# Kernel optimization log

Measured on AMD Instinct MI355X. Metric: run time of the kernel, lower is better.

The kernel has to match this reference:

```python
import jax, jax.numpy as jnp
import numpy as np

N = 50000      # nodes
E = 800000     # edges
F_IN = 128     # n_features
H = 4          # n_heads
C1 = 64        # n_hidden (per-head out of layer 1)
C2 = 32        # n_classes (per-head out of layer 2)
NEG_SLOPE = 0.2
EPS = 1e-16


def setup_inputs() -> dict:
    key = jax.random.key(0)
    ks = jax.random.split(key, 12)
    x = jax.random.normal(ks[0], (N, F_IN), dtype=jnp.float32)
    edge_index = jax.random.randint(ks[1], (2, E), 0, N, dtype=jnp.int64)
    # layer 1 params (GATConv: shared lin for src/dst, att_src/att_dst vectors, bias)
    W1 = jax.random.normal(ks[2], (F_IN, H * C1), dtype=jnp.float32) * (1.0 / np.sqrt(F_IN))
    att_src1 = jax.random.normal(ks[3], (H, C1), dtype=jnp.float32) * 0.1
    att_dst1 = jax.random.normal(ks[4], (H, C1), dtype=jnp.float32) * 0.1
    b1 = jnp.zeros((C1,), dtype=jnp.float32)
    # layer 2 params
    W2 = jax.random.normal(ks[5], (C1, H * C2), dtype=jnp.float32) * (1.0 / np.sqrt(C1))
    att_src2 = jax.random.normal(ks[6], (H, C2), dtype=jnp.float32) * 0.1
    att_dst2 = jax.random.normal(ks[7], (H, C2), dtype=jnp.float32) * 0.1
    b2 = jnp.zeros((C2,), dtype=jnp.float32)
    return {"x": x, "edge_index": edge_index,
            "W1": W1, "att_src1": att_src1, "att_dst1": att_dst1, "b1": b1,
            "W2": W2, "att_src2": att_src2, "att_dst2": att_dst2, "b2": b2}


def gat_conv(x, src, dst, W, att_src, att_dst, b, heads, out_ch):
    """PyG GATConv with concat=False (head-averaged output)."""
    n = x.shape[0]
    h = (x @ W).reshape(n, heads, out_ch)                 # [N, H, C]
    a_s = jnp.einsum('nhc,hc->nh', h, att_src)            # [N, H]
    a_d = jnp.einsum('nhc,hc->nh', h, att_dst)            # [N, H]
    e = jax.nn.leaky_relu(a_s[src] + a_d[dst], NEG_SLOPE)  # [E, H]
    # segment softmax over edges grouped by destination node
    m = jax.ops.segment_max(e, dst, num_segments=n)        # [N, H]
    m = jnp.where(jnp.isfinite(m), m, 0.0)
    ex = jnp.exp(e - m[dst])                               # [E, H]
    denom = jax.ops.segment_sum(ex, dst, num_segments=n)   # [N, H]
    alpha = ex / (denom[dst] + EPS)                        # [E, H]
    # scatter-add aggregation of attended source features
    msg = alpha[:, :, None] * h[src]                       # [E, H, C]
    out = jax.ops.segment_sum(msg, dst, num_segments=n)    # [N, H, C]
    return out.mean(axis=1) + b                            # [N, C]


def reference(x, edge_index, W1, att_src1, att_dst1, b1, W2, att_src2, att_dst2, b2):
    src, dst = edge_index[0], edge_index[1]
    h = jax.nn.relu(gat_conv(x, src, dst, W1, att_src1, att_dst1, b1, H, C1))
    # dropout is identity in eval mode
    out = gat_conv(h, src, dst, W2, att_src2, att_dst2, b2, H, C2)
    return out
```

## Files before the change

kernel.cpp:

```cpp
#include <hip/hip_runtime.h>
#include <hip/hip_fp16.h>
#include <cstdint>
#include <cstddef>

#define N_NODES 50000
#define N_EDGES 800000
#define F_IN 128
#define H_HEADS 4
#define C1 64
#define C2 32
#define NEG_SLOPE 0.2f
#define EPS_GAT 1e-16f
#define SLOT_CAP 96
#define FILL_BPG 256
#define NODES_PER_GROUP 6250
#define GEMM1_BLOCKS 782
#define CBASE ((int)0xAAAAAAAAu)

typedef _Float16 half8 __attribute__((ext_vector_type(8)));
typedef float f32x4 __attribute__((ext_vector_type(4)));

template<int K, int M>
__device__ __forceinline__ void wtrans_dev(const float* __restrict__ W,
                                           _Float16* __restrict__ Wt,
                                           _Float16* tile, int bm, int bk) {
    const int m0 = bm * 64, k0 = bk * 64;
    const int t = threadIdx.x;
    const int c = t & 63;
#pragma unroll
    for (int j = 0; j < 16; ++j) {
        int r = (t >> 6) + 4 * j;
        tile[c * 66 + r] = (_Float16)W[(size_t)(k0 + r) * M + m0 + c];
    }
    __syncthreads();
#pragma unroll
    for (int j = 0; j < 16; ++j) {
        int m_l = (t >> 6) + 4 * j;
        Wt[(size_t)(m0 + m_l) * K + k0 + c] = tile[m_l * 66 + c];
    }
}

__global__ __launch_bounds__(256) void wtrans_kernel(
        const float* __restrict__ W1, _Float16* __restrict__ wt1,
        const float* __restrict__ W2, _Float16* __restrict__ wt2) {
    __shared__ _Float16 tile[64 * 66];
    const int b = blockIdx.x;
    if (b < 8) {
        wtrans_dev<F_IN, H_HEADS * C1>(W1, wt1, tile, b & 3, b >> 2);
    } else {
        wtrans_dev<C1, H_HEADS * C2>(W2, wt2, tile, b - 8, 0);
    }
}

__device__ __forceinline__ void fill_dev(
        const int* __restrict__ src, const int* __restrict__ dst,
        int* __restrict__ cursor, unsigned short* __restrict__ slots,
        int fb) {
    const int g = (fb + (GEMM1_BLOCKS & 7)) & 7;
    const int bg = fb >> 3;
    const int dlo = g * NODES_PER_GROUP;
    const int dhi = dlo + NODES_PER_GROUP;
    const int4* dst4 = (const int4*)dst;
    const int4* src4 = (const int4*)src;
    constexpr int NV4 = N_EDGES / 4;
    for (int v = bg * 256 + (int)threadIdx.x; v < NV4; v += FILL_BPG * 256) {
        int4 d4 = dst4[v];
        int4 s4 = src4[v];
        if (d4.x >= dlo && d4.x < dhi) {
            unsigned int p = (unsigned int)(atomicAdd(&cursor[d4.x], 1) - CBASE);
            if (p < SLOT_CAP) slots[(size_t)d4.x * SLOT_CAP + p] = (unsigned short)s4.x;
        }
        if (d4.y >= dlo && d4.y < dhi) {
            unsigned int p = (unsigned int)(atomicAdd(&cursor[d4.y], 1) - CBASE);
            if (p < SLOT_CAP) slots[(size_t)d4.y * SLOT_CAP + p] = (unsigned short)s4.y;
        }
        if (d4.z >= dlo && d4.z < dhi) {
            unsigned int p = (unsigned int)(atomicAdd(&cursor[d4.z], 1) - CBASE);
            if (p < SLOT_CAP) slots[(size_t)d4.z * SLOT_CAP + p] = (unsigned short)s4.z;
        }
        if (d4.w >= dlo && d4.w < dhi) {
            unsigned int p = (unsigned int)(atomicAdd(&cursor[d4.w], 1) - CBASE);
            if (p < SLOT_CAP) slots[(size_t)d4.w * SLOT_CAP + p] = (unsigned short)s4.w;
        }
    }
}

template<int K, int M, int Hn, int C, typename InT>
__device__ __forceinline__ void gemm_att_dev(
        const InT* __restrict__ X, const _Float16* __restrict__ Wt,
        _Float16* __restrict__ Hout,
        const float* __restrict__ atts, const float* __restrict__ attd,
        float* __restrict__ as_, float* __restrict__ ad_, int Nr,
        _Float16* Ah, _Float16* Bt, _Float16* Ht, int row0) {
    constexpr int LDK = K + 8;
    constexpr int NCT = M / 64;
    constexpr int HPB = 64 / C;
    const int t = threadIdx.x;
    const int wv = t >> 6;
    const int lane = t & 63;
    const int quad = lane >> 4;
    const int n16 = lane & 15;

    if constexpr (sizeof(InT) == 4) {
        constexpr int KQ = K / 4;
#pragma unroll
        for (int j = 0; j < (64 * KQ) / 256; ++j) {
            int flat = t + 256 * j;
            int r = flat / KQ, kq = flat % KQ;
            int rg = row0 + r;
            float4 v = make_float4(0.f, 0.f, 0.f, 0.f);
            if (rg < Nr) v = *(const float4*)&X[(size_t)rg * K + 4 * kq];
            _Float16 tmp[4] = {(_Float16)v.x, (_Float16)v.y, (_Float16)v.z, (_Float16)v.w};
            *(uint2*)&Ah[r * LDK + 4 * kq] = *(const uint2*)tmp;
        }
    } else {
        constexpr int KQ = K / 8;
#pragma unroll
        for (int j = 0; j < (64 * KQ) / 256; ++j) {
            int flat = t + 256 * j;
            int r = flat / KQ, kq = flat % KQ;
            int rg = row0 + r;
            uint4 v = make_uint4(0u, 0u, 0u, 0u);
            if (rg < Nr) v = *(const uint4*)&X[(size_t)rg * K + 8 * kq];
            *(uint4*)&Ah[r * LDK + 8 * kq] = v;
        }
    }
    __syncthreads();

    half8 af[K / 32];
    const _Float16* Ap = &Ah[(16 * wv + n16) * LDK + 8 * quad];
#pragma unroll
    for (int ki = 0; ki < K / 32; ++ki) af[ki] = *(const half8*)(Ap + 32 * ki);

    for (int ct = 0; ct < NCT; ++ct) {
        const int col0 = 64 * ct;
        __syncthreads();
        {
            constexpr int KQ8 = K / 8;
#pragma unroll
            for (int j = 0; j < (64 * KQ8) / 256; ++j) {
                int flat = t + 256 * j;
                int c = flat / KQ8, kq = flat % KQ8;
                uint4 v = *(const uint4*)&Wt[(size_t)(col0 + c) * K + 8 * kq];
                *(uint4*)&Bt[c * LDK + 8 * kq] = v;
            }
        }
        __syncthreads();

        f32x4 acc[4];
#pragma unroll
        for (int nf = 0; nf < 4; ++nf) acc[nf] = (f32x4){0.f, 0.f, 0.f, 0.f};
#pragma unroll
        for (int ki = 0; ki < K / 32; ++ki) {
#pragma unroll
            for (int nf = 0; nf < 4; ++nf) {
                half8 bf = *(const half8*)&Bt[(16 * nf + n16) * LDK + 32 * ki + 8 * quad];
                acc[nf] = __builtin_amdgcn_mfma_f32_16x16x32_f16(af[ki], bf, acc[nf], 0, 0, 0);
            }
        }

        float dps[HPB][4], dpd[HPB][4];
#pragma unroll
        for (int u = 0; u < HPB; ++u)
#pragma unroll
            for (int r = 0; r < 4; ++r) { dps[u][r] = 0.f; dpd[u][r] = 0.f; }
#pragma unroll
        for (int nf = 0; nf < 4; ++nf) {
            int gc = col0 + 16 * nf + n16;
            float cs = atts[gc], cd = attd[gc];
#pragma unroll
            for (int r = 0; r < 4; ++r) {
                float av = acc[nf][r];
                dps[(16 * nf) / C][r] += av * cs;
                dpd[(16 * nf) / C][r] += av * cd;
            }
        }
#pragma unroll
        for (int u = 0; u < HPB; ++u)
#pragma unroll
            for (int r = 0; r < 4; ++r) {
                float s = dps[u][r], d = dpd[u][r];
#pragma unroll
                for (int off = 1; off < 16; off <<= 1) {
                    s += __shfl_xor(s, off, 64);
                    d += __shfl_xor(d, off, 64);
                }
                dps[u][r] = s; dpd[u][r] = d;
            }
        if (n16 == 0) {
            const int h0 = col0 / C;
#pragma unroll
            for (int r = 0; r < 4; ++r) {
                int row = row0 + 16 * wv + 4 * quad + r;
                if (row < Nr) {
#pragma unroll
                    for (int u = 0; u < HPB; ++u) {
                        as_[row * Hn + h0 + u] = dps[u][r];
                        ad_[row * Hn + h0 + u] = dpd[u][r];
                    }
                }
            }
        }

#pragma unroll
        for (int nf = 0; nf < 4; ++nf)
#pragma unroll
            for (int r = 0; r < 4; ++r)
                Ht[(16 * wv + 4 * quad + r) * 72 + 16 * nf + n16] = (_Float16)acc[nf][r];
        __syncthreads();
#pragma unroll
        for (int j = 0; j < 2; ++j) {
            int chunk = t + 256 * j;
            int r = chunk >> 3, cc = chunk & 7;
            int row = row0 + r;
            if (row < Nr) {
                uint4 v = *(const uint4*)&Ht[r * 72 + 8 * cc];
                *(uint4*)&Hout[(size_t)row * M + col0 + 8 * cc] = v;
            }
        }
    }
}

__global__ __launch_bounds__(256) void gemm1_fill_kernel(
        const float* __restrict__ x, const _Float16* __restrict__ wt1,
        _Float16* __restrict__ h1,
        const float* __restrict__ atts, const float* __restrict__ attd,
        float* __restrict__ as_, float* __restrict__ ad_,
        const int* __restrict__ src, const int* __restrict__ dst,
        int* __restrict__ cursor, unsigned short* __restrict__ slots) {
    constexpr int LDK = F_IN + 8;
    __shared__ _Float16 Ah[64 * LDK];
    __shared__ _Float16 Bt[64 * LDK];
    __shared__ _Float16 Ht[64 * 72];
    if (blockIdx.x < GEMM1_BLOCKS) {
        gemm_att_dev<F_IN, H_HEADS * C1, H_HEADS, C1, float>(
            x, wt1, h1, atts, attd, as_, ad_, N_NODES,
            Ah, Bt, Ht, blockIdx.x * 64);
    } else {
        fill_dev(src, dst, cursor, slots, blockIdx.x - GEMM1_BLOCKS);
    }
}

template<int K, int M, int Hn, int C, typename InT>
__global__ __launch_bounds__(256) void gemm_att_kernel(
        const InT* __restrict__ X, const _Float16* __restrict__ Wt,
        _Float16* __restrict__ Hout,
        const float* __restrict__ atts, const float* __restrict__ attd,
        float* __restrict__ as_, float* __restrict__ ad_, int Nr) {
    constexpr int LDK = K + 8;
    __shared__ _Float16 Ah[64 * LDK];
    __shared__ _Float16 Bt[64 * LDK];
    __shared__ _Float16 Ht[64 * 72];
    gemm_att_dev<K, M, Hn, C, InT>(X, Wt, Hout, atts, attd, as_, ad_, Nr,
                                   Ah, Bt, Ht, blockIdx.x * 64);
}

template<int Hn, int C, bool RELU, bool OUT_F16>
__global__ __launch_bounds__(256) void gat_agg_kernel(
        const int* __restrict__ degp, const unsigned short* __restrict__ slots,
        const float* __restrict__ as_, const float* __restrict__ ad_,
        const _Float16* __restrict__ Hm, const float* __restrict__ bias,
        void* __restrict__ outv, int Nr) {
    constexpr int HC = Hn * C;
    constexpr int PER = HC / 16;
    constexpr int NV = PER / 8;
    int node = blockIdx.x * 4 + (threadIdx.x >> 6);
    int lane = threadIdx.x & 63;
    if (node >= Nr) return;
    const int g = lane >> 4;
    const int l = lane & 15;
    const int h = l >> 2;
    const float ad_h = ad_[node * Hn + h];

    const int dn = min(degp[node] - CBASE, SLOT_CAP);
    const int begin = node * SLOT_CAP;
    const int end = begin + dn;
    const int iters = (dn + 3) >> 2;

    float acc[PER];
#pragma unroll
    for (int t = 0; t < PER; ++t) acc[t] = 0.f;
    float wsum = 0.f;

    int idx = begin + g;
    bool okA = idx < end;
    int sA = (int)slots[okA ? idx : begin];
    float aA = as_[sA * Hn + h];
    uint4 uA[NV];
    {
        const uint4* hp = (const uint4*)(Hm + (size_t)sA * HC + l * PER);
        uA[0] = hp[0];
        if constexpr (NV == 2) uA[1] = hp[1];
    }

#pragma unroll 2
    for (int it = 0; it < iters; ++it) {
        const int j = idx + 4;
        const bool okB = j < end;
        int sB = (int)slots[okB ? j : begin];
        float aB = as_[sB * Hn + h];
        uint4 uB[NV];
        {
            const uint4* hp = (const uint4*)(Hm + (size_t)sB * HC + l * PER);
            uB[0] = hp[0];
            if constexpr (NV == 2) uB[1] = hp[1];
        }

        float logit = aA + ad_h;
        float lr = fmaxf(logit, NEG_SLOPE * logit);
        float w = okA ? __expf(lr) : 0.f;
        wsum += w;
#pragma unroll
        for (int v = 0; v < NV; ++v) {
            half8 hv = __builtin_bit_cast(half8, uA[v]);
#pragma unroll
            for (int e = 0; e < 8; ++e)
                acc[8 * v + e] = fmaf((float)hv[e], w, acc[8 * v + e]);
        }

        okA = okB; aA = aB;
        uA[0] = uB[0];
        if constexpr (NV == 2) uA[1] = uB[1];
        idx = j;
    }

#pragma unroll
    for (int t = 0; t < PER; ++t) {
        acc[t] += __shfl_xor(acc[t], 16, 64);
        acc[t] += __shfl_xor(acc[t], 32, 64);
    }
    wsum += __shfl_xor(wsum, 16, 64);
    wsum += __shfl_xor(wsum, 32, 64);
    const float inv = 1.f / (wsum + EPS_GAT);
    float val[PER];
#pragma unroll
    for (int t = 0; t < PER; ++t) {
        float v = acc[t] * inv;
        v += __shfl_xor(v, 4, 64);
        v += __shfl_xor(v, 8, 64);
        val[t] = v * (1.0f / Hn);
    }
    if (lane < 4) {
        const int c0 = lane * PER;
#pragma unroll
        for (int t = 0; t < PER; ++t) {
            float v = val[t] + bias[c0 + t];
            if (RELU) v = fmaxf(v, 0.f);
            val[t] = v;
        }
        if constexpr (OUT_F16) {
            _Float16* o = (_Float16*)outv;
            _Float16 tmp[PER];
#pragma unroll
            for (int t = 0; t < PER; ++t) tmp[t] = (_Float16)val[t];
            uint4* d4 = (uint4*)&o[(size_t)node * C + c0];
            d4[0] = *(const uint4*)&tmp[0];
            if constexpr (NV == 2) d4[1] = *(const uint4*)&tmp[8];
        } else {
            float* o = (float*)outv;
#pragma unroll
            for (int t4 = 0; t4 < PER / 4; ++t4)
                *(float4*)&o[(size_t)node * C + c0 + 4 * t4] =
                    make_float4(val[4 * t4 + 0], val[4 * t4 + 1],
                                val[4 * t4 + 2], val[4 * t4 + 3]);
        }
    }
}

extern "C" void kernel_launch(void* const* d_in, const int* in_sizes, int n_in,
                              void* d_out, int out_size, void* d_ws, size_t ws_size,
                              hipStream_t stream) {
    const float* x    = (const float*)d_in[0];
    const int*   ei   = (const int*)d_in[1];
    const float* W1   = (const float*)d_in[2];
    const float* as1w = (const float*)d_in[3];
    const float* ad1w = (const float*)d_in[4];
    const float* b1   = (const float*)d_in[5];
    const float* W2   = (const float*)d_in[6];
    const float* as2w = (const float*)d_in[7];
    const float* ad2w = (const float*)d_in[8];
    const float* b2   = (const float*)d_in[9];
    float* out = (float*)d_out;

    const int* src = ei;
    const int* dst = ei + N_EDGES;

    char* ws = (char*)d_ws;
    size_t off = 0;
    auto alloc = [&](size_t bytes) -> void* {
        void* p = ws + off;
        off = (off + bytes + 255) & ~(size_t)255;
        return p;
    };
    int*   cursor = (int*)alloc((size_t)N_NODES * 4);
    float* as1_ = (float*)alloc((size_t)N_NODES * H_HEADS * 4);
    float* ad1_ = (float*)alloc((size_t)N_NODES * H_HEADS * 4);
    float* as2_ = (float*)alloc((size_t)N_NODES * H_HEADS * 4);
    float* ad2_ = (float*)alloc((size_t)N_NODES * H_HEADS * 4);
    _Float16* h1   = (_Float16*)alloc((size_t)N_NODES * H_HEADS * C1 * 2);
    _Float16* out1 = (_Float16*)alloc((size_t)N_NODES * C1 * 2);
    _Float16* h2   = (_Float16*)alloc((size_t)N_NODES * H_HEADS * C2 * 2);
    _Float16* wt1  = (_Float16*)alloc((size_t)(H_HEADS * C1) * F_IN * 2);
    _Float16* wt2  = (_Float16*)alloc((size_t)(H_HEADS * C2) * C1 * 2);
    unsigned short* slots = (unsigned short*)alloc((size_t)N_NODES * SLOT_CAP * 2);

    wtrans_kernel<<<10, 256, 0, stream>>>(W1, wt1, W2, wt2);

    gemm1_fill_kernel<<<GEMM1_BLOCKS + 8 * FILL_BPG, 256, 0, stream>>>(
        x, wt1, h1, as1w, ad1w, as1_, ad1_, src, dst, cursor, slots);

    gat_agg_kernel<H_HEADS, C1, true, true><<<(N_NODES + 3) / 4, 256, 0, stream>>>(
        cursor, slots, as1_, ad1_, h1, b1, (void*)out1, N_NODES);

    gemm_att_kernel<C1, H_HEADS * C2, H_HEADS, C2, _Float16>
        <<<GEMM1_BLOCKS, 256, 0, stream>>>(
            out1, wt2, h2, as2w, ad2w, as2_, ad2_, N_NODES);

    gat_agg_kernel<H_HEADS, C2, false, false><<<(N_NODES + 3) / 4, 256, 0, stream>>>(
        cursor, slots, as2_, ad2_, h2, b2, (void*)out, N_NODES);
}
```

Before: 239.3 us.

## Read GEMM weights directly from global and alias LDS to raise occupancy

The GEMM+attention device routine no longer stages weight tiles through shared memory. MFMA B fragments are loaded straight from global (L2/L1-cached) weights, and the output staging tile reuses the A buffer. This cuts LDS per block to one buffer and removes a barrier per column tile, and launch bounds now request 6 blocks per SIMD-group for higher occupancy. The cost is uncoalesced per-lane global reads of weights in the inner loop, plus possible register pressure from the occupancy hint. Reusing the A buffer for output staging is safe only because the A fragments are already held in registers.

```diff
diff --git a/kernel.cpp b/kernel.cpp
--- a/kernel.cpp
+++ b/kernel.cpp
@@ -91,7 +91,7 @@
         _Float16* __restrict__ Hout,
         const float* __restrict__ atts, const float* __restrict__ attd,
         float* __restrict__ as_, float* __restrict__ ad_, int Nr,
-        _Float16* Ah, _Float16* Bt, _Float16* Ht, int row0) {
+        _Float16* SA, int row0) {
     constexpr int LDK = K + 8;
     constexpr int NCT = M / 64;
     constexpr int HPB = 64 / C;
@@ -111,7 +111,7 @@
             float4 v = make_float4(0.f, 0.f, 0.f, 0.f);
             if (rg < Nr) v = *(const float4*)&X[(size_t)rg * K + 4 * kq];
             _Float16 tmp[4] = {(_Float16)v.x, (_Float16)v.y, (_Float16)v.z, (_Float16)v.w};
-            *(uint2*)&Ah[r * LDK + 4 * kq] = *(const uint2*)tmp;
+            *(uint2*)&SA[r * LDK + 4 * kq] = *(const uint2*)tmp;
         }
     } else {
         constexpr int KQ = K / 8;
@@ -122,31 +122,23 @@
             int rg = row0 + r;
             uint4 v = make_uint4(0u, 0u, 0u, 0u);
             if (rg < Nr) v = *(const uint4*)&X[(size_t)rg * K + 8 * kq];
-            *(uint4*)&Ah[r * LDK + 8 * kq] = v;
+            *(uint4*)&SA[r * LDK + 8 * kq] = v;
         }
     }
     __syncthreads();
 
     half8 af[K / 32];
-    const _Float16* Ap = &Ah[(16 * wv + n16) * LDK + 8 * quad];
+    const _Float16* Ap = &SA[(16 * wv + n16) * LDK + 8 * quad];
 #pragma unroll
     for (int ki = 0; ki < K / 32; ++ki) af[ki] = *(const half8*)(Ap + 32 * ki);
+
+    _Float16* Ht = SA;
 
     for (int ct = 0; ct < NCT; ++ct) {
         const int col0 = 64 * ct;
         __syncthreads();
-        {
-            constexpr int KQ8 = K / 8;
-#pragma unroll
-            for (int j = 0; j < (64 * KQ8) / 256; ++j) {
-                int flat = t + 256 * j;
-                int c = flat / KQ8, kq = flat % KQ8;
-                uint4 v = *(const uint4*)&Wt[(size_t)(col0 + c) * K + 8 * kq];
-                *(uint4*)&Bt[c * LDK + 8 * kq] = v;
-            }
-        }
-        __syncthreads();
-
+
+        const _Float16* Bp = Wt + (size_t)(col0 + n16) * K + 8 * quad;
         f32x4 acc[4];
 #pragma unroll
         for (int nf = 0; nf < 4; ++nf) acc[nf] = (f32x4){0.f, 0.f, 0.f, 0.f};
@@ -154,7 +146,7 @@
         for (int ki = 0; ki < K / 32; ++ki) {
 #pragma unroll
             for (int nf = 0; nf < 4; ++nf) {
-                half8 bf = *(const half8*)&Bt[(16 * nf + n16) * LDK + 32 * ki + 8 * quad];
+                half8 bf = *(const half8*)(Bp + (size_t)(16 * nf) * K + 32 * ki);
                 acc[nf] = __builtin_amdgcn_mfma_f32_16x16x32_f16(af[ki], bf, acc[nf], 0, 0, 0);
             }
         }
@@ -221,38 +213,31 @@
     }
 }
 
-__global__ __launch_bounds__(256) void gemm1_fill_kernel(
+__global__ __launch_bounds__(256, 6) void gemm1_fill_kernel(
         const float* __restrict__ x, const _Float16* __restrict__ wt1,
         _Float16* __restrict__ h1,
         const float* __restrict__ atts, const float* __restrict__ attd,
         float* __restrict__ as_, float* __restrict__ ad_,
         const int* __restrict__ src, const int* __restrict__ dst,
         int* __restrict__ cursor, unsigned short* __restrict__ slots) {
-    constexpr int LDK = F_IN + 8;
-    __shared__ _Float16 Ah[64 * LDK];
-    __shared__ _Float16 Bt[64 * LDK];
-    __shared__ _Float16 Ht[64 * 72];
+    __shared__ _Float16 SA[64 * (F_IN + 8)];
     if (blockIdx.x < GEMM1_BLOCKS) {
         gemm_att_dev<F_IN, H_HEADS * C1, H_HEADS, C1, float>(
-            x, wt1, h1, atts, attd, as_, ad_, N_NODES,
-            Ah, Bt, Ht, blockIdx.x * 64);
+            x, wt1, h1, atts, attd, as_, ad_, N_NODES, SA, blockIdx.x * 64);
     } else {
         fill_dev(src, dst, cursor, slots, blockIdx.x - GEMM1_BLOCKS);
     }
 }
 
 template<int K, int M, int Hn, int C, typename InT>
-__global__ __launch_bounds__(256) void gemm_att_kernel(
+__global__ __launch_bounds__(256, 6) void gemm_att_kernel(
         const InT* __restrict__ X, const _Float16* __restrict__ Wt,
         _Float16* __restrict__ Hout,
         const float* __restrict__ atts, const float* __restrict__ attd,
         float* __restrict__ as_, float* __restrict__ ad_, int Nr) {
-    constexpr int LDK = K + 8;
-    __shared__ _Float16 Ah[64 * LDK];
-    __shared__ _Float16 Bt[64 * LDK];
-    __shared__ _Float16 Ht[64 * 72];
+    __shared__ _Float16 SA[64 * (K + 8)];
     gemm_att_dev<K, M, Hn, C, InT>(X, Wt, Hout, atts, attd, as_, ad_, Nr,
-                                   Ah, Bt, Ht, blockIdx.x * 64);
+                                   SA, blockIdx.x * 64);
 }
 
 template<int Hn, int C, bool RELU, bool OUT_F16>
```

Result: slower. 245.5 us (+2.6%).

## Fuse layer-1 aggregation with layer-2 linear transform and attention logits

Applied to the files above, without the earlier changes.

Replaces the separate layer-1 aggregation kernel and the layer-2 GEMM kernel with one kernel. After each wavefront aggregates a node's 64-dim output, it multiplies by W2 in registers using per-lane dot products and shuffles, then writes h2 and the attention scalars directly. This removes the out1 intermediate round-trip through memory and one kernel launch. The cost is scalar FMA matvec work in place of MFMA GEMM, extra shuffles, and repeated W2 reads per node, which may raise register pressure.

```diff
diff --git a/kernel.cpp b/kernel.cpp
--- a/kernel.cpp
+++ b/kernel.cpp
@@ -241,18 +241,141 @@
     }
 }
 
-template<int K, int M, int Hn, int C, typename InT>
-__global__ __launch_bounds__(256) void gemm_att_kernel(
-        const InT* __restrict__ X, const _Float16* __restrict__ Wt,
-        _Float16* __restrict__ Hout,
-        const float* __restrict__ atts, const float* __restrict__ attd,
-        float* __restrict__ as_, float* __restrict__ ad_, int Nr) {
-    constexpr int LDK = K + 8;
-    __shared__ _Float16 Ah[64 * LDK];
-    __shared__ _Float16 Bt[64 * LDK];
-    __shared__ _Float16 Ht[64 * 72];
-    gemm_att_dev<K, M, Hn, C, InT>(X, Wt, Hout, atts, attd, as_, ad_, Nr,
-                                   Ah, Bt, Ht, blockIdx.x * 64);
+__global__ __launch_bounds__(256) void agg1_mv_kernel(
+        const int* __restrict__ degp, const unsigned short* __restrict__ slots,
+        const float* __restrict__ as_, const float* __restrict__ ad_,
+        const _Float16* __restrict__ Hm, const float* __restrict__ bias,
+        const _Float16* __restrict__ wt2,
+        const float* __restrict__ atts2, const float* __restrict__ attd2,
+        _Float16* __restrict__ h2, float* __restrict__ as2_,
+        float* __restrict__ ad2_, int Nr) {
+    constexpr int Hn = H_HEADS;
+    constexpr int HC = Hn * C1;
+    constexpr int PER = 16;
+    int node = blockIdx.x * 4 + (threadIdx.x >> 6);
+    int lane = threadIdx.x & 63;
+    if (node >= Nr) return;
+    const int g = lane >> 4;
+    const int l = lane & 15;
+    const int h = l >> 2;
+    const float ad_h = ad_[node * Hn + h];
+
+    const int dn = min(degp[node] - CBASE, SLOT_CAP);
+    const int begin = node * SLOT_CAP;
+    const int end = begin + dn;
+    const int iters = (dn + 3) >> 2;
+
+    float acc[PER];
+#pragma unroll
+    for (int t = 0; t < PER; ++t) acc[t] = 0.f;
+    float wsum = 0.f;
+
+    int idx = begin + g;
+    bool okA = idx < end;
+    int sA = (int)slots[okA ? idx : begin];
+    float aA = as_[sA * Hn + h];
+    uint4 uA[2];
+    {
+        const uint4* hp = (const uint4*)(Hm + (size_t)sA * HC + l * PER);
+        uA[0] = hp[0]; uA[1] = hp[1];
+    }
+
+#pragma unroll 2
+    for (int it = 0; it < iters; ++it) {
+        const int j = idx + 4;
+        const bool okB = j < end;
+        int sB = (int)slots[okB ? j : begin];
+        float aB = as_[sB * Hn + h];
+        uint4 uB[2];
+        {
+            const uint4* hp = (const uint4*)(Hm + (size_t)sB * HC + l * PER);
+            uB[0] = hp[0]; uB[1] = hp[1];
+        }
+
+        float logit = aA + ad_h;
+        float lr = fmaxf(logit, NEG_SLOPE * logit);
+        float w = okA ? __expf(lr) : 0.f;
+        wsum += w;
+#pragma unroll
+        for (int v = 0; v < 2; ++v) {
+            half8 hv = __builtin_bit_cast(half8, uA[v]);
+#pragma unroll
+            for (int e = 0; e < 8; ++e)
+                acc[8 * v + e] = fmaf((float)hv[e], w, acc[8 * v + e]);
+        }
+        okA = okB; aA = aB; uA[0] = uB[0]; uA[1] = uB[1];
+        idx = j;
+    }
+
+#pragma unroll
+    for (int t = 0; t < PER; ++t) {
+        acc[t] += __shfl_xor(acc[t], 16, 64);
+        acc[t] += __shfl_xor(acc[t], 32, 64);
+    }
+    wsum += __shfl_xor(wsum, 16, 64);
+    wsum += __shfl_xor(wsum, 32, 64);
+    const float inv = 1.f / (wsum + EPS_GAT);
+    const int q = lane & 3;
+    float val[PER];
+#pragma unroll
+    for (int t = 0; t < PER; ++t) {
+        float v = acc[t] * inv;
+        v += __shfl_xor(v, 4, 64);
+        v += __shfl_xor(v, 8, 64);
+        v = v * (1.0f / Hn) + bias[q * PER + t];
+        val[t] = fmaxf(v, 0.f);
+    }
+
+    const int r = lane >> 2;
+    float p[8];
+#pragma unroll
+    for (int k = 0; k < 8; ++k) {
+        const _Float16* wrow = wt2 + (size_t)(r + 16 * k) * C1 + q * PER;
+        half8 wa = *(const half8*)wrow;
+        half8 wb = *(const half8*)(wrow + 8);
+        float s = 0.f;
+#pragma unroll
+        for (int e = 0; e < 8; ++e) s = fmaf((float)wa[e], val[e], s);
+#pragma unroll
+        for (int e = 0; e < 8; ++e) s = fmaf((float)wb[e], val[8 + e], s);
+        p[k] = s;
+    }
+#pragma unroll
+    for (int k = 0; k < 8; ++k) {
+        p[k] += __shfl_xor(p[k], 1, 64);
+        p[k] += __shfl_xor(p[k], 2, 64);
+    }
+
+    float asum[4], adsum[4];
+#pragma unroll
+    for (int hh = 0; hh < 4; ++hh) {
+        int m0 = r + 32 * hh, m1 = m0 + 16;
+        float a = p[2 * hh] * atts2[m0] + p[2 * hh + 1] * atts2[m1];
+        float d = p[2 * hh] * attd2[m0] + p[2 * hh + 1] * attd2[m1];
+        asum[hh] = (q == 0) ? a : 0.f;
+        adsum[hh] = (q == 0) ? d : 0.f;
+    }
+#pragma unroll
+    for (int hh = 0; hh < 4; ++hh) {
+#pragma unroll
+        for (int off = 1; off < 64; off <<= 1) {
+            asum[hh] += __shfl_xor(asum[hh], off, 64);
+            adsum[hh] += __shfl_xor(adsum[hh], off, 64);
+        }
+    }
+    if (lane == 0) {
+#pragma unroll
+        for (int hh = 0; hh < 4; ++hh) {
+            as2_[node * Hn + hh] = asum[hh];
+            ad2_[node * Hn + hh] = adsum[hh];
+        }
+    }
+
+    if (q == 0) {
+        _Float16* hp = h2 + (size_t)node * (H_HEADS * C2);
+#pragma unroll
+        for (int k = 0; k < 8; ++k) hp[r + 16 * k] = (_Float16)p[k];
+    }
 }
 
 template<int Hn, int C, bool RELU, bool OUT_F16>
@@ -317,7 +440,6 @@
             for (int e = 0; e < 8; ++e)
                 acc[8 * v + e] = fmaf((float)hv[e], w, acc[8 * v + e]);
         }
-
         okA = okB; aA = aB;
         uA[0] = uB[0];
         if constexpr (NV == 2) uA[1] = uB[1];
@@ -398,7 +520,6 @@
     float* as2_ = (float*)alloc((size_t)N_NODES * H_HEADS * 4);
     float* ad2_ = (float*)alloc((size_t)N_NODES * H_HEADS * 4);
     _Float16* h1   = (_Float16*)alloc((size_t)N_NODES * H_HEADS * C1 * 2);
-    _Float16* out1 = (_Float16*)alloc((size_t)N_NODES * C1 * 2);
     _Float16* h2   = (_Float16*)alloc((size_t)N_NODES * H_HEADS * C2 * 2);
     _Float16* wt1  = (_Float16*)alloc((size_t)(H_HEADS * C1) * F_IN * 2);
     _Float16* wt2  = (_Float16*)alloc((size_t)(H_HEADS * C2) * C1 * 2);
@@ -409,12 +530,9 @@
     gemm1_fill_kernel<<<GEMM1_BLOCKS + 8 * FILL_BPG, 256, 0, stream>>>(
         x, wt1, h1, as1w, ad1w, as1_, ad1_, src, dst, cursor, slots);
 
-    gat_agg_kernel<H_HEADS, C1, true, true><<<(N_NODES + 3) / 4, 256, 0, stream>>>(
-        cursor, slots, as1_, ad1_, h1, b1, (void*)out1, N_NODES);
-
-    gemm_att_kernel<C1, H_HEADS * C2, H_HEADS, C2, _Float16>
-        <<<GEMM1_BLOCKS, 256, 0, stream>>>(
-            out1, wt2, h2, as2w, ad2w, as2_, ad2_, N_NODES);
+    agg1_mv_kernel<<<(N_NODES + 3) / 4, 256, 0, stream>>>(
+        cursor, slots, as1_, ad1_, h1, b1, wt2, as2w, ad2w,
+        h2, as2_, ad2_, N_NODES);
 
     gat_agg_kernel<H_HEADS, C2, false, false><<<(N_NODES + 3) / 4, 256, 0, stream>>>(
         cursor, slots, as2_, ad2_, h2, b2, (void*)out, N_NODES);
```

After: 262.4 us. 1.1x slower.

## Overlap second half of layer-1 aggregation with layer-2 GEMM on first half

Applied to the files above, without the earlier changes.

Layer-1 aggregation is split at a node boundary. The first half runs alone. The second half is fused into one launch together with the layer-2 GEMM for rows already produced by the first half, and a separate kernel then runs the GEMM on the remaining rows. The goal is to fill the GPU's idle tail and hide the GEMM behind the memory-bound aggregation, at the cost of an extra launch and a fused kernel with tighter launch bounds that shares LDS.

```diff
diff --git a/kernel.cpp b/kernel.cpp
--- a/kernel.cpp
+++ b/kernel.cpp
@@ -15,6 +15,11 @@
 #define FILL_BPG 256
 #define NODES_PER_GROUP 6250
 #define GEMM1_BLOCKS 782
+#define SPLIT_NODES 25024
+#define AGG1A_BLOCKS 6256
+#define AGG1B_BLOCKS 6244
+#define GEMM2A_RB 391
+#define GEMM2B_BLOCKS 391
 #define CBASE ((int)0xAAAAAAAAu)
 
 typedef _Float16 half8 __attribute__((ext_vector_type(8)));
@@ -91,9 +96,8 @@
         _Float16* __restrict__ Hout,
         const float* __restrict__ atts, const float* __restrict__ attd,
         float* __restrict__ as_, float* __restrict__ ad_, int Nr,
-        _Float16* Ah, _Float16* Bt, _Float16* Ht, int row0) {
+        _Float16* Ah, _Float16* Bt, _Float16* Ht, int row0, int ct0, int nct) {
     constexpr int LDK = K + 8;
-    constexpr int NCT = M / 64;
     constexpr int HPB = 64 / C;
     const int t = threadIdx.x;
     const int wv = t >> 6;
@@ -132,7 +136,7 @@
 #pragma unroll
     for (int ki = 0; ki < K / 32; ++ki) af[ki] = *(const half8*)(Ap + 32 * ki);
 
-    for (int ct = 0; ct < NCT; ++ct) {
+    for (int ct = ct0; ct < ct0 + nct; ++ct) {
         const int col0 = 64 * ct;
         __syncthreads();
         {
@@ -235,38 +239,21 @@
     if (blockIdx.x < GEMM1_BLOCKS) {
         gemm_att_dev<F_IN, H_HEADS * C1, H_HEADS, C1, float>(
             x, wt1, h1, atts, attd, as_, ad_, N_NODES,
-            Ah, Bt, Ht, blockIdx.x * 64);
+            Ah, Bt, Ht, blockIdx.x * 64, 0, 4);
     } else {
         fill_dev(src, dst, cursor, slots, blockIdx.x - GEMM1_BLOCKS);
     }
 }
 
-template<int K, int M, int Hn, int C, typename InT>
-__global__ __launch_bounds__(256) void gemm_att_kernel(
-        const InT* __restrict__ X, const _Float16* __restrict__ Wt,
-        _Float16* __restrict__ Hout,
-        const float* __restrict__ atts, const float* __restrict__ attd,
-        float* __restrict__ as_, float* __restrict__ ad_, int Nr) {
-    constexpr int LDK = K + 8;
-    __shared__ _Float16 Ah[64 * LDK];
-    __shared__ _Float16 Bt[64 * LDK];
-    __shared__ _Float16 Ht[64 * 72];
-    gemm_att_dev<K, M, Hn, C, InT>(X, Wt, Hout, atts, attd, as_, ad_, Nr,
-                                   Ah, Bt, Ht, blockIdx.x * 64);
-}
-
 template<int Hn, int C, bool RELU, bool OUT_F16>
-__global__ __launch_bounds__(256) void gat_agg_kernel(
+__device__ __forceinline__ void gat_agg_dev(
         const int* __restrict__ degp, const unsigned short* __restrict__ slots,
         const float* __restrict__ as_, const float* __restrict__ ad_,
         const _Float16* __restrict__ Hm, const float* __restrict__ bias,
-        void* __restrict__ outv, int Nr) {
+        void* __restrict__ outv, int node, int lane) {
     constexpr int HC = Hn * C;
     constexpr int PER = HC / 16;
     constexpr int NV = PER / 8;
-    int node = blockIdx.x * 4 + (threadIdx.x >> 6);
-    int lane = threadIdx.x & 63;
-    if (node >= Nr) return;
     const int g = lane >> 4;
     const int l = lane & 15;
     const int h = l >> 2;
@@ -317,7 +304,6 @@
             for (int e = 0; e < 8; ++e)
                 acc[8 * v + e] = fmaf((float)hv[e], w, acc[8 * v + e]);
         }
-
         okA = okB; aA = aB;
         uA[0] = uB[0];
         if constexpr (NV == 2) uA[1] = uB[1];
@@ -365,6 +351,54 @@
                                 val[4 * t4 + 2], val[4 * t4 + 3]);
         }
     }
+}
+
+template<int Hn, int C, bool RELU, bool OUT_F16>
+__global__ __launch_bounds__(256) void gat_agg_kernel(
+        const int* __restrict__ degp, const unsigned short* __restrict__ slots,
+        const float* __restrict__ as_, const float* __restrict__ ad_,
+        const _Float16* __restrict__ Hm, const float* __restrict__ bias,
+        void* __restrict__ outv, int node0, int Nr) {
+    int node = node0 + blockIdx.x * 4 + (threadIdx.x >> 6);
+    if (node >= Nr) return;
+    gat_agg_dev<Hn, C, RELU, OUT_F16>(degp, slots, as_, ad_, Hm, bias, outv,
+                                      node, threadIdx.x & 63);
+}
+
+__global__ __launch_bounds__(256, 8) void agg1b_gemm2a_kernel(
+        const int* __restrict__ degp, const unsigned short* __restrict__ slots,
+        const float* __restrict__ as1_, const float* __restrict__ ad1_,
+        const _Float16* __restrict__ h1, const float* __restrict__ b1,
+        _Float16* __restrict__ out1,
+        const _Float16* __restrict__ wt2,
+        const float* __restrict__ as2w, const float* __restrict__ ad2w,
+        _Float16* __restrict__ h2, float* __restrict__ as2_,
+        float* __restrict__ ad2_) {
+    __shared__ _Float16 SAB[2 * 64 * 72];
+    if (blockIdx.x < AGG1B_BLOCKS) {
+        int node = SPLIT_NODES + blockIdx.x * 4 + (threadIdx.x >> 6);
+        gat_agg_dev<H_HEADS, C1, true, true>(
+            degp, slots, as1_, ad1_, h1, b1, (void*)out1,
+            node, threadIdx.x & 63);
+    } else {
+        int rb = blockIdx.x - AGG1B_BLOCKS;
+        gemm_att_dev<C1, H_HEADS * C2, H_HEADS, C2, _Float16>(
+            out1, wt2, h2, as2w, ad2w, as2_, ad2_, N_NODES,
+            SAB, SAB + 64 * 72, SAB, rb * 64, 0, 2);
+    }
+}
+
+__global__ __launch_bounds__(256) void gemm2b_kernel(
+        const _Float16* __restrict__ out1, const _Float16* __restrict__ wt2,
+        _Float16* __restrict__ h2,
+        const float* __restrict__ as2w, const float* __restrict__ ad2w,
+        float* __restrict__ as2_, float* __restrict__ ad2_) {
+    __shared__ _Float16 Ah[64 * 72];
+    __shared__ _Float16 Bt[64 * 72];
+    int rb = GEMM2A_RB + blockIdx.x;
+    gemm_att_dev<C1, H_HEADS * C2, H_HEADS, C2, _Float16>(
+        out1, wt2, h2, as2w, ad2w, as2_, ad2_, N_NODES,
+        Ah, Bt, Ah, rb * 64, 0, 2);
 }
 
 extern "C" void kernel_launch(void* const* d_in, const int* in_sizes, int n_in,
@@ -409,13 +443,16 @@
     gemm1_fill_kernel<<<GEMM1_BLOCKS + 8 * FILL_BPG, 256, 0, stream>>>(
         x, wt1, h1, as1w, ad1w, as1_, ad1_, src, dst, cursor, slots);
 
-    gat_agg_kernel<H_HEADS, C1, true, true><<<(N_NODES + 3) / 4, 256, 0, stream>>>(
-        cursor, slots, as1_, ad1_, h1, b1, (void*)out1, N_NODES);
-
-    gemm_att_kernel<C1, H_HEADS * C2, H_HEADS, C2, _Float16>
-        <<<GEMM1_BLOCKS, 256, 0, stream>>>(
-            out1, wt2, h2, as2w, ad2w, as2_, ad2_, N_NODES);
+    gat_agg_kernel<H_HEADS, C1, true, true><<<AGG1A_BLOCKS, 256, 0, stream>>>(
+        cursor, slots, as1_, ad1_, h1, b1, (void*)out1, 0, SPLIT_NODES);
+
+    agg1b_gemm2a_kernel<<<AGG1B_BLOCKS + GEMM2A_RB, 256, 0, stream>>>(
+        cursor, slots, as1_, ad1_, h1, b1, out1,
+        wt2, as2w, ad2w, h2, as2_, ad2_);
+
+    gemm2b_kernel<<<GEMM2B_BLOCKS, 256, 0, stream>>>(
+        out1, wt2, h2, as2w, ad2w, as2_, ad2_);
 
     gat_agg_kernel<H_HEADS, C2, false, false><<<(N_NODES + 3) / 4, 256, 0, stream>>>(
-        cursor, slots, as2_, ad2_, h2, b2, (void*)out, N_NODES);
-}
+        cursor, slots, as2_, ad2_, h2, b2, (void*)out, 0, N_NODES);
+}
```

New measurement: 256.8 us. 7.3% more time.
